# Performance work log

Measured on AMD Instinct MI355X. Metric: run time of the kernel, lower is better.

Reference implementation:

```python
import jax, jax.numpy as jnp
import numpy as np

B, S, D_IN, H, G, C, E = 16, 1024, 128, 256, 256, 17, 524288
N = B * S  # nodes = batch*seq, as in the torch view()


def setup_inputs() -> dict:
    key = jax.random.key(0)
    ks = jax.random.split(key, 20)
    s_l = 1.0 / np.sqrt(H)
    def u(k, shape, s):
        return jax.random.uniform(k, shape, jnp.float32, -s, s)
    return {
        "x": jax.random.normal(ks[0], (B, S, D_IN), jnp.float32),
        "edge_index": jax.random.randint(ks[1], (2, E), 0, N, jnp.int64),
        "w_ih_f": u(ks[2], (4 * H, D_IN), s_l),
        "w_hh_f": u(ks[3], (4 * H, H), s_l),
        "b_ih_f": u(ks[4], (4 * H,), s_l),
        "b_hh_f": u(ks[5], (4 * H,), s_l),
        "w_ih_r": u(ks[6], (4 * H, D_IN), s_l),
        "w_hh_r": u(ks[7], (4 * H, H), s_l),
        "b_ih_r": u(ks[8], (4 * H,), s_l),
        "b_hh_r": u(ks[9], (4 * H,), s_l),
        "W1": u(ks[10], (2 * H, G), 1.0 / np.sqrt(2 * H)),
        "b1": jnp.zeros((G,), jnp.float32),
        "W2": u(ks[11], (G, G), 1.0 / np.sqrt(G)),
        "b2": jnp.zeros((G,), jnp.float32),
        "Wc": u(ks[12], (G, C), 1.0 / np.sqrt(G)),
        "bc": jnp.zeros((C,), jnp.float32),
    }


def _lstm_dir(x, w_ih, w_hh, b_ih, b_hh, reverse):
    # x: [B,S,D]; precompute input contribution: [S,B,4H]
    xg = jnp.einsum("bsd,gd->sbg", x, w_ih) + (b_ih + b_hh)
    h0 = jnp.zeros((x.shape[0], H), x.dtype)
    def step(carry, xt):
        h, c = carry
        gates = xt + h @ w_hh.T
        i, f, g, o = jnp.split(gates, 4, axis=-1)  # torch gate order i,f,g,o
        i, f, o = jax.nn.sigmoid(i), jax.nn.sigmoid(f), jax.nn.sigmoid(o)
        c = f * c + i * jnp.tanh(g)
        h = o * jnp.tanh(c)
        return (h, c), h
    _, hs = jax.lax.scan(step, (h0, h0), xg, reverse=reverse)
    return jnp.transpose(hs, (1, 0, 2))  # [B,S,H]


def _gcn(x, W, b, src, dst):
    # PyG GCNConv: transform, add self-loops, symmetric norm, scatter-add, bias
    h = x @ W  # [N,G]
    deg = jax.ops.segment_sum(jnp.ones(src.shape[0], h.dtype), dst, num_segments=N)
    inv = jax.lax.rsqrt(jnp.maximum(deg, 1e-12))
    msg = h[src] * (inv[src] * inv[dst])[:, None]
    return jax.ops.segment_sum(msg, dst, num_segments=N) + b


def reference(x, edge_index, w_ih_f, w_hh_f, b_ih_f, b_hh_f,
              w_ih_r, w_hh_r, b_ih_r, b_hh_r, W1, b1, W2, b2, Wc, bc):
    hf = _lstm_dir(x, w_ih_f, w_hh_f, b_ih_f, b_hh_f, reverse=False)
    hr = _lstm_dir(x, w_ih_r, w_hh_r, b_ih_r, b_hh_r, reverse=True)
    nodes = jnp.concatenate([hf, hr], axis=-1).reshape(N, 2 * H)
    loop = jnp.arange(N, dtype=edge_index.dtype)
    src = jnp.concatenate([edge_index[0], loop])
    dst = jnp.concatenate([edge_index[1], loop])
    g = jax.nn.relu(_gcn(nodes, W1, b1, src, dst))
    g = jax.nn.relu(_gcn(g, W2, b2, src, dst))
    logits = g @ Wc + bc
    return logits.reshape(B, S, C)
```

## Files before the change

kernel.cpp:

```cpp
#include <hip/hip_runtime.h>
#include <hip/hip_bf16.h>
#include <hip/hip_fp16.h>
#include <cstdint>
#include <cstddef>

#define B_  16
#define S_  1024
#define DIN 128
#define H_  256
#define G4  1024
#define GD  256
#define CD  17
#define E_  524288
#define N_  16384

typedef _Float16 f16;
typedef _Float16 f16x2 __attribute__((ext_vector_type(2)));
typedef _Float16 f16x8 __attribute__((ext_vector_type(8)));
typedef float    f32x4 __attribute__((ext_vector_type(4)));

#define DOT2(a, b, c) __builtin_amdgcn_fdot2((a), (b), (c), false)

__device__ __forceinline__ float sigf(float x) { return 1.0f / (1.0f + __expf(-x)); }
__device__ __forceinline__ float tanhfast(float x) { return 1.0f - 2.0f / (__expf(2.0f * x) + 1.0f); }

__global__ void sentinel_kernel(float* out, float v) {
    out[blockIdx.x * 256 + threadIdx.x] = v;
}

__global__ void count_kernel(const int* __restrict__ ei, int* __restrict__ cnt) {
    int i = blockIdx.x * 256 + threadIdx.x;
    atomicAdd(&cnt[ei[E_ + i]], 1);
}

__global__ void scan_kernel(const int* __restrict__ cnt, int* __restrict__ offs) {
    __shared__ int sums[1024];
    const int t = threadIdx.x;
    int loc[16];
    int s = 0;
    const int base = t * 16;
#pragma unroll
    for (int i = 0; i < 16; i++) { loc[i] = cnt[base + i]; s += loc[i]; }
    sums[t] = s;
    __syncthreads();
    for (int d = 1; d < 1024; d <<= 1) {
        int v = 0;
        if (t >= d) v = sums[t - d];
        __syncthreads();
        if (t >= d) sums[t] += v;
        __syncthreads();
    }
    int ex = (t == 0) ? 0 : sums[t - 1];
#pragma unroll
    for (int i = 0; i < 16; i++) { offs[base + i] = ex; ex += loc[i]; }
    if (t == 1023) offs[N_] = ex;
}

__global__ void fill_kernel(const int* __restrict__ ei, const int* __restrict__ offs,
                            int* __restrict__ cursor, int* __restrict__ csr) {
    int i = blockIdx.x * 256 + threadIdx.x;
    int dv = ei[E_ + i];
    int p = atomicAdd(&cursor[dv], 1);
    csr[offs[dv] + p] = ei[i];
}

__global__ void inv_kernel(const int* __restrict__ cnt, float* __restrict__ invd) {
    int n = blockIdx.x * 256 + threadIdx.x;
    invd[n] = rsqrtf((float)(cnt[n] + 1));
}

__global__ void cvt16_kernel(const float* __restrict__ src, f16* __restrict__ dst, int n) {
    int i = blockIdx.x * 256 + threadIdx.x;
    if (i < n) dst[i] = (f16)src[i];
}

__global__ void bias_comb_kernel(const float* __restrict__ a, const float* __restrict__ b,
                                 float* __restrict__ o) {
    int i = blockIdx.x * 256 + threadIdx.x;
    o[i] = a[i] + b[i];
}

template <int K>
__global__ void wsplit_kernel(const float* __restrict__ W, f16* __restrict__ hi,
                              f16* __restrict__ lo) {
    int idx = blockIdx.x * 256 + threadIdx.x;
    int k = idx >> 8, n = idx & 255;
    float v = W[idx];
    f16 h = (f16)v;
    hi[(size_t)n * K + k] = h;
    lo[(size_t)n * K + k] = (f16)(v - (float)h);
}

template <int K, bool BIAS, bool RESID, typename OutT>
__global__ __launch_bounds__(256)
void mgemm_kernel(const f16* __restrict__ A, const f16* __restrict__ BT,
                  const f16* __restrict__ BTlo, const float* __restrict__ bias,
                  OutT* __restrict__ C, int ldc)
{
    const int wv = threadIdx.x >> 6, lane = threadIdx.x & 63;
    const int m0 = blockIdx.x * 64 + wv * 16;
    const int n0 = blockIdx.y * 256;
    const int rw = lane & 15, kq = lane >> 4;
    f32x4 acc[16];
#pragma unroll
    for (int t = 0; t < 16; ++t) acc[t] = (f32x4){0.f, 0.f, 0.f, 0.f};

    const f16* __restrict__ Ap = A + (size_t)(m0 + rw) * K + kq * 8;
    for (int k0 = 0; k0 < K; k0 += 32) {
        const f16x8 a = *(const f16x8*)(Ap + k0);
#pragma unroll
        for (int t = 0; t < 16; ++t) {
            const size_t boff = (size_t)(n0 + t * 16 + rw) * K + k0 + kq * 8;
            acc[t] = __builtin_amdgcn_mfma_f32_16x16x32_f16(a, *(const f16x8*)(BT + boff), acc[t], 0, 0, 0);
            if constexpr (RESID) {
                acc[t] = __builtin_amdgcn_mfma_f32_16x16x32_f16(a, *(const f16x8*)(BTlo + boff), acc[t], 0, 0, 0);
            }
        }
    }
    const int orow = m0 + kq * 4;
#pragma unroll
    for (int t = 0; t < 16; ++t) {
        const int col = n0 + t * 16 + rw;
        float bv = 0.f;
        if constexpr (BIAS) bv = bias[col];
#pragma unroll
        for (int r = 0; r < 4; ++r) {
            C[(size_t)(orow + r) * ldc + col] = (OutT)(acc[t][r] + bv);
        }
    }
}

__global__ __launch_bounds__(512, 2)
void lstm_kernel(const f16* __restrict__ xg,
                 const float* __restrict__ whh_f, const float* __restrict__ whh_r,
                 f16* __restrict__ nodes)
{
    __shared__ __align__(16) f16x2 gw[256 * 2 * 64];
    __shared__ __align__(16) f16 hbuf[2][256];

    const int t = threadIdx.x;
    const int u = t >> 1, kh = t & 1;
    const int u7 = u & 7;
    const int d = blockIdx.x >> 4, b = blockIdx.x & 15;
    const float* __restrict__ whh = d ? whh_r : whh_f;

    f16x2 wr[3][64];
    {
        const int rws[3] = {u, 256 + u, 768 + u};
#pragma unroll
        for (int r = 0; r < 3; r++) {
            const float* src = whh + (size_t)rws[r] * H_ + kh * 128;
#pragma unroll
            for (int c = 0; c < 64; c++) {
                f16x2 w; w[0] = (f16)src[2 * c]; w[1] = (f16)src[2 * c + 1];
                wr[r][c] = w;
            }
        }
    }
    {
        const float* src = whh + (size_t)(512 + u) * H_ + kh * 128;
        f16x2* dst = gw + (u * 2 + kh) * 64;
#pragma unroll
        for (int lw = 0; lw < 64; ++lw) {
            int phys = (((lw >> 2) ^ u7) << 2) | (lw & 3);
            f16x2 w; w[0] = (f16)src[2 * lw]; w[1] = (f16)src[2 * lw + 1];
            dst[phys] = w;
        }
    }
    if (t < 256) { hbuf[0][t] = (f16)0.f; hbuf[1][t] = (f16)0.f; }
    __syncthreads();

    float c_st = 0.f;
    const f16* xgb = xg + ((size_t)(d * B_ + b)) * S_ * G4;
    f16* nb = nodes + (size_t)b * S_ * 512 + d * H_;

    for (int si = 0; si < S_; ++si) {
        const int s = d ? (S_ - 1 - si) : si;
        const int cur = si & 1;

        const f16* xr = xgb + (size_t)s * G4 + u;
        const float xi = (float)xr[0];
        const float xf = (float)xr[256];
        const float xg_ = (float)xr[512];
        const float xo = (float)xr[768];

        float a0 = 0.f, a1 = 0.f, a2 = 0.f, a3 = 0.f;
        float a4 = 0.f, a5 = 0.f, a6 = 0.f, a7 = 0.f;
        const f16x8* hp = (const f16x8*)&hbuf[cur][kh * 128];
        const f16x8* gp = (const f16x8*)(gw + (u * 2 + kh) * 64);

#pragma unroll
        for (int c = 0; c < 4; c++) {
#pragma unroll
            for (int j = 0; j < 4; j++) {
                f16x8 hv = hp[c * 4 + j];
                f16x8 gv = gp[(c * 4 + j) ^ u7];
#pragma unroll
                for (int p = 0; p < 4; p++) {
                    f16x2 h2; h2[0] = hv[2 * p]; h2[1] = hv[2 * p + 1];
                    f16x2 g2; g2[0] = gv[2 * p]; g2[1] = gv[2 * p + 1];
                    const int w = c * 16 + j * 4 + p;
                    if (p & 1) {
                        a1 = DOT2(h2, wr[0][w], a1);
                        a3 = DOT2(h2, wr[1][w], a3);
                        a5 = DOT2(h2, wr[2][w], a5);
                        a7 = DOT2(h2, g2, a7);
                    } else {
                        a0 = DOT2(h2, wr[0][w], a0);
                        a2 = DOT2(h2, wr[1][w], a2);
                        a4 = DOT2(h2, wr[2][w], a4);
                        a6 = DOT2(h2, g2, a6);
                    }
                }
            }
        }
        float ti = a0 + a1, tf = a2 + a3, to = a4 + a5, tg = a6 + a7;
        ti += __shfl_xor(ti, 1);
        tf += __shfl_xor(tf, 1);
        to += __shfl_xor(to, 1);
        tg += __shfl_xor(tg, 1);

        const float ig = sigf(xi + ti);
        const float fg = sigf(xf + tf);
        const float gt = tanhfast(xg_ + tg);
        const float og = sigf(xo + to);
        c_st = fg * c_st + ig * gt;
        const float h = og * tanhfast(c_st);
        const f16 hfv = (f16)h;

        if (kh == 0) {
            hbuf[cur ^ 1][u] = hfv;
            nb[(size_t)s * 512 + u] = hfv;
        }
        __syncthreads();
    }
}

template <typename OutT>
__global__ __launch_bounds__(256)
void gather_kernel(const float* __restrict__ Hm, const int* __restrict__ csr,
                   const int* __restrict__ offs, const float* __restrict__ inv,
                   const float* __restrict__ bias, OutT* __restrict__ Out) {
    const int wid = threadIdx.x >> 6, lane = threadIdx.x & 63;
    const int n = blockIdx.x * 4 + wid;
    const float invn = inv[n];
    const float4* __restrict__ H4 = (const float4*)Hm;

    float4 v = H4[(size_t)n * 64 + lane];
    const float sw = invn * invn;
    float ax = v.x * sw, ay = v.y * sw, az = v.z * sw, aw = v.w * sw;

    const int e0 = offs[n], e1 = offs[n + 1];
    for (int e = e0; e < e1; ++e) {
        const int src = csr[e];
        const float w = inv[src] * invn;
        float4 hv = H4[(size_t)src * 64 + lane];
        ax = fmaf(hv.x, w, ax);
        ay = fmaf(hv.y, w, ay);
        az = fmaf(hv.z, w, az);
        aw = fmaf(hv.w, w, aw);
    }
    const float4 bv = ((const float4*)bias)[lane];
    OutT* o = Out + (size_t)n * GD + lane * 4;
    o[0] = (OutT)fmaxf(ax + bv.x, 0.f);
    o[1] = (OutT)fmaxf(ay + bv.y, 0.f);
    o[2] = (OutT)fmaxf(az + bv.z, 0.f);
    o[3] = (OutT)fmaxf(aw + bv.w, 0.f);
}

__global__ __launch_bounds__(256)
void cls_kernel(const float* __restrict__ g2, const float* __restrict__ Wc,
                const float* __restrict__ bc, float* __restrict__ out) {
    const int idx = blockIdx.x * 256 + threadIdx.x;
    if (idx >= N_ * CD) return;
    const int n = idx / CD, c = idx % CD;
    const float* __restrict__ row = g2 + (size_t)n * GD;
    float a0 = bc[c], a1 = 0.f, a2 = 0.f, a3 = 0.f;
    for (int k = 0; k < GD; k += 4) {
        a0 = fmaf(row[k + 0], Wc[(size_t)(k + 0) * CD + c], a0);
        a1 = fmaf(row[k + 1], Wc[(size_t)(k + 1) * CD + c], a1);
        a2 = fmaf(row[k + 2], Wc[(size_t)(k + 2) * CD + c], a2);
        a3 = fmaf(row[k + 3], Wc[(size_t)(k + 3) * CD + c], a3);
    }
    out[idx] = (a0 + a1) + (a2 + a3);
}

extern "C" void kernel_launch(void* const* d_in, const int* in_sizes, int n_in,
                              void* d_out, int out_size, void* d_ws, size_t ws_size,
                              hipStream_t stream) {
    const float* x     = (const float*)d_in[0];
    const int*   ei    = (const int*)d_in[1];
    const float* wih_f = (const float*)d_in[2];
    const float* whh_f = (const float*)d_in[3];
    const float* bih_f = (const float*)d_in[4];
    const float* bhh_f = (const float*)d_in[5];
    const float* wih_r = (const float*)d_in[6];
    const float* whh_r = (const float*)d_in[7];
    const float* bih_r = (const float*)d_in[8];
    const float* bhh_r = (const float*)d_in[9];
    const float* W1    = (const float*)d_in[10];
    const float* b1    = (const float*)d_in[11];
    const float* W2    = (const float*)d_in[12];
    const float* b2    = (const float*)d_in[13];
    const float* Wc    = (const float*)d_in[14];
    const float* bc    = (const float*)d_in[15];
    float* out = (float*)d_out;
    (void)out_size;

    static const int EXP_SIZES[16] = {
        2097152, 1048576, 131072, 262144, 1024, 1024,
        131072, 262144, 1024, 1024, 131072, 256, 65536, 256, 4352, 17
    };
    if (n_in != 16) { sentinel_kernel<<<4, 256, 0, stream>>>(out, 3.5e6f); return; }
    for (int i = 0; i < 16; ++i) {
        if (in_sizes[i] != EXP_SIZES[i]) {
            sentinel_kernel<<<4, 256, 0, stream>>>(out, 1.0e6f + (float)(i + 1) * 1.0e5f);
            return;
        }
    }

    char* ws = (char*)d_ws;
    size_t off = 0;
    auto alloc = [&](size_t bytes) -> char* {
        char* p = ws + off;
        off = (off + bytes + 255) & ~(size_t)255;
        return p;
    };
    f16*   xg     = (f16*)  alloc((size_t)2 * B_ * S_ * G4 * sizeof(f16));
    f16*   nodes  = (f16*)  alloc((size_t)N_ * 512 * sizeof(f16));
    int*   cnt    = (int*)  alloc((size_t)N_ * 4);
    float* invd   = (float*)alloc((size_t)N_ * 4);
    int*   offs   = (int*)  alloc((size_t)(N_ + 1) * 4);
    int*   cursor = (int*)  alloc((size_t)N_ * 4);
    int*   csr    = (int*)  alloc((size_t)E_ * 4);
    const size_t NEED = off;

    char* nreg = (char*)nodes;
    f16*   xf16   = (f16*)  (nreg);
    f16*   wih16f = (f16*)  (nreg + 4300800);
    f16*   wih16r = (f16*)  (nreg + 4300800 + 270336);
    float* biasf  = (float*)(nreg + 4300800 + 2 * 270336);
    float* biasr  = (float*)(nreg + 4300800 + 2 * 270336 + 8192);

    char* xreg = (char*)xg;
    float* h1 = (float*)(xreg);
    f16*   g1 = (f16*)  (xreg + 16777216);
    float* g2 = (float*)(xreg + 16777216 + 8388608);
    f16*   W1Thi = (f16*)(xreg + 50331648);
    f16*   W1Tlo = (f16*)(xreg + 50331648 + 262144);
    f16*   W2Thi = (f16*)(xreg + 50331648 + 2 * 262144);
    f16*   W2Tlo = (f16*)(xreg + 50331648 + 2 * 262144 + 131072);

    if (ws_size < NEED) {
        sentinel_kernel<<<4, 256, 0, stream>>>(out, 1.0e6f + 1000.0f * (float)(ws_size >> 20));
        return;
    }

    hipMemsetAsync(cnt, 0, (size_t)N_ * 4, stream);
    hipMemsetAsync(cursor, 0, (size_t)N_ * 4, stream);

    count_kernel<<<E_ / 256, 256, 0, stream>>>(ei, cnt);
    scan_kernel<<<1, 1024, 0, stream>>>(cnt, offs);
    fill_kernel<<<E_ / 256, 256, 0, stream>>>(ei, offs, cursor, csr);
    inv_kernel<<<N_ / 256, 256, 0, stream>>>(cnt, invd);

    cvt16_kernel<<<(2097152 + 255) / 256, 256, 0, stream>>>(x, xf16, 2097152);
    cvt16_kernel<<<(131072 + 255) / 256, 256, 0, stream>>>(wih_f, wih16f, 131072);
    cvt16_kernel<<<(131072 + 255) / 256, 256, 0, stream>>>(wih_r, wih16r, 131072);
    bias_comb_kernel<<<4, 256, 0, stream>>>(bih_f, bhh_f, biasf);
    bias_comb_kernel<<<4, 256, 0, stream>>>(bih_r, bhh_r, biasr);

    mgemm_kernel<128, true, false, f16><<<dim3(256, 4), 256, 0, stream>>>(
        xf16, wih16f, nullptr, biasf, xg, G4);
    mgemm_kernel<128, true, false, f16><<<dim3(256, 4), 256, 0, stream>>>(
        xf16, wih16r, nullptr, biasr, xg + (size_t)B_ * S_ * G4, G4);

    lstm_kernel<<<32, 512, 0, stream>>>(xg, whh_f, whh_r, nodes);

    wsplit_kernel<512><<<512 * 256 / 256, 256, 0, stream>>>(W1, W1Thi, W1Tlo);
    wsplit_kernel<256><<<256 * 256 / 256, 256, 0, stream>>>(W2, W2Thi, W2Tlo);

    mgemm_kernel<512, false, true, float><<<dim3(256, 1), 256, 0, stream>>>(
        nodes, W1Thi, W1Tlo, nullptr, h1, GD);
    gather_kernel<f16><<<N_ / 4, 256, 0, stream>>>(h1, csr, offs, invd, b1, g1);
    mgemm_kernel<256, false, true, float><<<dim3(256, 1), 256, 0, stream>>>(
        g1, W2Thi, W2Tlo, nullptr, h1, GD);
    gather_kernel<float><<<N_ / 4, 256, 0, stream>>>(h1, csr, offs, invd, b2, g2);
    cls_kernel<<<(N_ * CD + 255) / 256, 256, 0, stream>>>(g2, Wc, bc, out);
}
```

Before: 2.360 ms.

## Split LSTM recurrence across four threads per hidden unit, one gate each

Restructures the LSTM recurrent kernel from 512 threads (two threads per hidden unit, each holding three gate rows in registers plus one gate row in LDS) to 1024 threads where each thread owns one full gate row of W_hh in registers. Each thread does a 256-long dot product against the shared h vector, and the four gate values of a unit are exchanged with xor shuffles. This removes the LDS-resident weight reads and the cross-half reduction, and shortens the per-step serial dot-product chain. In exchange it doubles the threads per block and raises register pressure under a 1024-thread launch bound, and the block-wide barrier now spans twice as many waves.

Result: slower. 3.713 ms (+57.3%).

```diff
diff --git a/kernel.cpp b/kernel.cpp
--- a/kernel.cpp
+++ b/kernel.cpp
@@ -130,107 +130,77 @@
     }
 }
 
-__global__ __launch_bounds__(512, 2)
+__global__ __launch_bounds__(1024, 1)
 void lstm_kernel(const f16* __restrict__ xg,
                  const float* __restrict__ whh_f, const float* __restrict__ whh_r,
                  f16* __restrict__ nodes)
 {
-    __shared__ __align__(16) f16x2 gw[256 * 2 * 64];
-    __shared__ __align__(16) f16 hbuf[2][256];
+    __shared__ __align__(16) f16 hb[2][256];
 
     const int t = threadIdx.x;
-    const int u = t >> 1, kh = t & 1;
-    const int u7 = u & 7;
+    const int u = t >> 2, gq = t & 3;
     const int d = blockIdx.x >> 4, b = blockIdx.x & 15;
     const float* __restrict__ whh = d ? whh_r : whh_f;
 
-    f16x2 wr[3][64];
+    f16x2 wv[128];
     {
-        const int rws[3] = {u, 256 + u, 768 + u};
-#pragma unroll
-        for (int r = 0; r < 3; r++) {
-            const float* src = whh + (size_t)rws[r] * H_ + kh * 128;
-#pragma unroll
-            for (int c = 0; c < 64; c++) {
-                f16x2 w; w[0] = (f16)src[2 * c]; w[1] = (f16)src[2 * c + 1];
-                wr[r][c] = w;
-            }
-        }
-    }
-    {
-        const float* src = whh + (size_t)(512 + u) * H_ + kh * 128;
-        f16x2* dst = gw + (u * 2 + kh) * 64;
-#pragma unroll
-        for (int lw = 0; lw < 64; ++lw) {
-            int phys = (((lw >> 2) ^ u7) << 2) | (lw & 3);
-            f16x2 w; w[0] = (f16)src[2 * lw]; w[1] = (f16)src[2 * lw + 1];
-            dst[phys] = w;
-        }
-    }
-    if (t < 256) { hbuf[0][t] = (f16)0.f; hbuf[1][t] = (f16)0.f; }
+        const float* src = whh + (size_t)(gq * 256 + u) * H_;
+#pragma unroll
+        for (int c = 0; c < 128; c++) {
+            f16x2 w; w[0] = (f16)src[2 * c]; w[1] = (f16)src[2 * c + 1];
+            wv[c] = w;
+        }
+    }
+    if (t < 256) { hb[0][t] = (f16)0.f; hb[1][t] = (f16)0.f; }
     __syncthreads();
 
     float c_st = 0.f;
-    const f16* xgb = xg + ((size_t)(d * B_ + b)) * S_ * G4;
-    f16* nb = nodes + (size_t)b * S_ * 512 + d * H_;
+    const f16* __restrict__ xgb = xg + ((size_t)(d * B_ + b)) * S_ * G4 + gq * 256 + u;
+    f16* __restrict__ nb = nodes + (size_t)b * S_ * 512 + d * H_ + u;
 
     for (int si = 0; si < S_; ++si) {
         const int s = d ? (S_ - 1 - si) : si;
         const int cur = si & 1;
 
-        const f16* xr = xgb + (size_t)s * G4 + u;
-        const float xi = (float)xr[0];
-        const float xf = (float)xr[256];
-        const float xg_ = (float)xr[512];
-        const float xo = (float)xr[768];
+        const float xv = (float)xgb[(size_t)s * G4];
 
         float a0 = 0.f, a1 = 0.f, a2 = 0.f, a3 = 0.f;
-        float a4 = 0.f, a5 = 0.f, a6 = 0.f, a7 = 0.f;
-        const f16x8* hp = (const f16x8*)&hbuf[cur][kh * 128];
-        const f16x8* gp = (const f16x8*)(gw + (u * 2 + kh) * 64);
-
-#pragma unroll
-        for (int c = 0; c < 4; c++) {
-#pragma unroll
-            for (int j = 0; j < 4; j++) {
-                f16x8 hv = hp[c * 4 + j];
-                f16x8 gv = gp[(c * 4 + j) ^ u7];
-#pragma unroll
-                for (int p = 0; p < 4; p++) {
-                    f16x2 h2; h2[0] = hv[2 * p]; h2[1] = hv[2 * p + 1];
-                    f16x2 g2; g2[0] = gv[2 * p]; g2[1] = gv[2 * p + 1];
-                    const int w = c * 16 + j * 4 + p;
-                    if (p & 1) {
-                        a1 = DOT2(h2, wr[0][w], a1);
-                        a3 = DOT2(h2, wr[1][w], a3);
-                        a5 = DOT2(h2, wr[2][w], a5);
-                        a7 = DOT2(h2, g2, a7);
-                    } else {
-                        a0 = DOT2(h2, wr[0][w], a0);
-                        a2 = DOT2(h2, wr[1][w], a2);
-                        a4 = DOT2(h2, wr[2][w], a4);
-                        a6 = DOT2(h2, g2, a6);
-                    }
-                }
-            }
-        }
-        float ti = a0 + a1, tf = a2 + a3, to = a4 + a5, tg = a6 + a7;
-        ti += __shfl_xor(ti, 1);
-        tf += __shfl_xor(tf, 1);
-        to += __shfl_xor(to, 1);
-        tg += __shfl_xor(tg, 1);
-
-        const float ig = sigf(xi + ti);
-        const float fg = sigf(xf + tf);
-        const float gt = tanhfast(xg_ + tg);
-        const float og = sigf(xo + to);
+        const f16x8* __restrict__ hp = (const f16x8*)&hb[cur][0];
+#pragma unroll
+        for (int c = 0; c < 32; c++) {
+            f16x8 hv = hp[c];
+            f16x2 h2;
+            h2[0] = hv[0]; h2[1] = hv[1];
+            a0 = DOT2(h2, wv[c * 4 + 0], a0);
+            h2[0] = hv[2]; h2[1] = hv[3];
+            a1 = DOT2(h2, wv[c * 4 + 1], a1);
+            h2[0] = hv[4]; h2[1] = hv[5];
+            a2 = DOT2(h2, wv[c * 4 + 2], a2);
+            h2[0] = hv[6]; h2[1] = hv[7];
+            a3 = DOT2(h2, wv[c * 4 + 3], a3);
+        }
+        const float own = ((a0 + a1) + (a2 + a3)) + xv;
+
+        const float s1 = __shfl_xor(own, 1);
+        const float s2 = __shfl_xor(own, 2);
+        const float s3 = __shfl_xor(s1, 2);
+        const bool b0 = (gq & 1) != 0, b1 = (gq & 2) != 0;
+        const float gi = b1 ? (b0 ? s3 : s2) : (b0 ? s1 : own);
+        const float gf = b1 ? (b0 ? s2 : s3) : (b0 ? own : s1);
+        const float gg = b1 ? (b0 ? s1 : own) : (b0 ? s3 : s2);
+        const float go = b1 ? (b0 ? own : s1) : (b0 ? s2 : s3);
+
+        const float ig = sigf(gi);
+        const float fg = sigf(gf);
+        const float gt = tanhfast(gg);
+        const float og = sigf(go);
         c_st = fg * c_st + ig * gt;
         const float h = og * tanhfast(c_st);
         const f16 hfv = (f16)h;
 
-        if (kh == 0) {
-            hbuf[cur ^ 1][u] = hfv;
-            nb[(size_t)s * 512 + u] = hfv;
+        if (gq == 0) {
+            hb[cur ^ 1][u] = hfv;
+            nb[(size_t)s * 512] = hfv;
         }
         __syncthreads();
     }
@@ -375,7 +345,7 @@
     mgemm_kernel<128, true, false, f16><<<dim3(256, 4), 256, 0, stream>>>(
         xf16, wih16r, nullptr, biasr, xg + (size_t)B_ * S_ * G4, G4);
 
-    lstm_kernel<<<32, 512, 0, stream>>>(xg, whh_f, whh_r, nodes);
+    lstm_kernel<<<32, 1024, 0, stream>>>(xg, whh_f, whh_r, nodes);
 
     wsplit_kernel<512><<<512 * 256 / 256, 256, 0, stream>>>(W1, W1Thi, W1Tlo);
     wsplit_kernel<256><<<256 * 256 / 256, 256, 0, stream>>>(W2, W2Thi, W2Tlo);
```
